# Kernel optimization log

Measured on AMD Instinct MI355X. Metric: run time of the kernel, lower is better.

Reference implementation:

```python
import jax, jax.numpy as jnp
import numpy as np


def _lovasz_softmax_flat(probas, labels):
    # probas: [P, C] softmax probabilities; labels: [P] int class ids
    P, C = probas.shape
    classes = jnp.arange(C)
    # fg[c, p] = 1 if pixel p has ground-truth class c
    fg = (labels[None, :] == classes[:, None]).astype(probas.dtype)      # [C, P]
    errors = jnp.abs(fg - probas.T)                                       # [C, P]
    # sort errors descending per class, permute fg the same way
    order = jnp.argsort(-errors, axis=1)                                  # [C, P]
    errors_sorted = jnp.take_along_axis(errors, order, axis=1)
    fg_sorted = jnp.take_along_axis(fg, order, axis=1)
    # Lovasz gradient of the Jaccard loss w.r.t. sorted errors
    gts = jnp.sum(fg_sorted, axis=1, keepdims=True)                       # [C, 1]
    intersection = gts - jnp.cumsum(fg_sorted, axis=1)
    union = gts + jnp.cumsum(1.0 - fg_sorted, axis=1)
    jaccard = 1.0 - intersection / union                                  # [C, P]
    jaccard = jnp.concatenate([jaccard[:, :1], jaccard[:, 1:] - jaccard[:, :-1]], axis=1)
    # grad is treated as constant w.r.t. probas (matches torch Variable(grad) detach)
    jaccard = jax.lax.stop_gradient(jaccard)
    losses = jnp.sum(errors_sorted * jaccard, axis=1)                     # [C]
    # classes='present': average only over classes present in the labels
    present = (gts[:, 0] > 0).astype(probas.dtype)
    return jnp.sum(losses * present) / jnp.maximum(jnp.sum(present), 1.0)


def reference(input, target):
    B, C, H, W = input.shape
    probas = jax.nn.softmax(input, axis=1)                                # [B, C, H, W]
    probas_flat = probas.transpose(0, 2, 3, 1).reshape(-1, C)             # [P, C]
    labels_flat = target.reshape(-1)                                      # [P]
    return _lovasz_softmax_flat(probas_flat, labels_flat)


def setup_inputs() -> dict:
    key = jax.random.key(0)
    k1, k2 = jax.random.split(key)
    B, C, H, W = 8, 19, 512, 512
    inp = jax.random.normal(k1, (B, C, H, W), dtype=jnp.float32)
    tgt = jax.random.randint(k2, (B, H, W), 0, C, dtype=jnp.int64)
    return {"input": inp, "target": tgt}
```

## Files before the change

### kernel.cpp

```cpp
#include <hip/hip_runtime.h>
#include <stdint.h>


#define C_CLASSES 19
#define NBINS 768
#define HISTWORDS (C_CLASSES * NBINS)
#define HW_SHIFT 18
#define HW_MASK ((1 << HW_SHIFT) - 1)
#define NGROUPS 8

__device__ __forceinline__ void px_process(float* r, float m, int lab,
                                           unsigned int* hist)
{
    float s = 0.f;
#pragma unroll
    for (int c = 0; c < C_CLASSES; ++c) {
        float t = __expf(r[c] - m);
        r[c] = t;
        s += t;
    }
    float scale = (float)(NBINS - 1) * __builtin_amdgcn_rcpf(s);
#pragma unroll
    for (int c = 0; c < C_CLASSES; ++c) {
        int ti = __float2int_rn(r[c] * scale);
        int idx = (c == lab) ? (NBINS - 1 - ti) : ti;
        idx = idx < 0 ? 0 : (idx > NBINS - 1 ? NBINS - 1 : idx);
        atomicAdd(&hist[c * NBINS + idx], (c == lab) ? 0x10001u : 1u);
    }
}

__global__ __launch_bounds__(1024) void k1_hist(
    const float* __restrict__ x, const int* __restrict__ labels,
    unsigned int* __restrict__ copies, int P, int pixPerBlk)
{
    __shared__ unsigned int hist[HISTWORDS];
    int tid = threadIdx.x;
    uint4* h4 = (uint4*)hist;
    for (int i = tid; i < HISTWORDS / 4; i += 1024) h4[i] = make_uint4(0u, 0u, 0u, 0u);
    __syncthreads();

    int base = blockIdx.x * pixPerBlk;
    for (int it = 0; it < pixPerBlk; it += 4096) {
        int pix = base + it + tid * 4;
        if (pix + 3 < P) {
            int img = pix >> HW_SHIFT;
            int rem = pix & HW_MASK;
            const float* xp = x + (((size_t)img * C_CLASSES) << HW_SHIFT) + rem;
            float r0[C_CLASSES], r1[C_CLASSES], r2[C_CLASSES], r3[C_CLASSES];
            float m0 = -3.4e38f, m1 = -3.4e38f, m2 = -3.4e38f, m3 = -3.4e38f;
#pragma unroll
            for (int c = 0; c < C_CLASSES; ++c) {
                float4 v = *reinterpret_cast<const float4*>(xp + ((size_t)c << HW_SHIFT));
                r0[c] = v.x; r1[c] = v.y; r2[c] = v.z; r3[c] = v.w;
                m0 = fmaxf(m0, v.x); m1 = fmaxf(m1, v.y);
                m2 = fmaxf(m2, v.z); m3 = fmaxf(m3, v.w);
            }
            int4 lb = *reinterpret_cast<const int4*>(labels + pix);
            px_process(r0, m0, lb.x, hist);
            px_process(r1, m1, lb.y, hist);
            px_process(r2, m2, lb.z, hist);
            px_process(r3, m3, lb.w, hist);
        } else {
#pragma unroll
            for (int k = 0; k < 4; ++k) {
                int p = pix + k;
                if (p < P) {
                    int img = p >> HW_SHIFT;
                    int rem = p & HW_MASK;
                    const float* xp = x + (((size_t)img * C_CLASSES) << HW_SHIFT) + rem;
                    float r[C_CLASSES];
                    float m = -3.4e38f;
#pragma unroll
                    for (int c = 0; c < C_CLASSES; ++c) {
                        r[c] = xp[(size_t)c << HW_SHIFT];
                        m = fmaxf(m, r[c]);
                    }
                    px_process(r, m, labels[p], hist);
                }
            }
        }
    }
    __syncthreads();
    uint4* dst = (uint4*)(copies + (size_t)blockIdx.x * HISTWORDS);
    const uint4* src = (const uint4*)hist;
    for (int i = tid; i < HISTWORDS / 4; i += 1024) dst[i] = src[i];
}

__global__ __launch_bounds__(256) void k2_reduce(
    const unsigned int* __restrict__ copies,
    int* __restrict__ nPart, int* __restrict__ fPart,
    int* __restrict__ ticket, int ncopies, int cpg)
{
    if (blockIdx.x == 0 && blockIdx.y == 0 && threadIdx.x == 0) *ticket = 0;
    int pos = blockIdx.x * 256 + threadIdx.x;
    int g = blockIdx.y;
    int c0 = g * cpg;
    int c1 = c0 + cpg; if (c1 > ncopies) c1 = ncopies;
    unsigned int sn = 0, sf = 0;
    for (int k = c0; k < c1; ++k) {
        unsigned int w = copies[(size_t)k * HISTWORDS + pos];
        sn += w & 0xFFFFu;
        sf += w >> 16;
    }
    nPart[(size_t)g * HISTWORDS + pos] = (int)sn;
    fPart[(size_t)g * HISTWORDS + pos] = (int)sf;
}

__global__ __launch_bounds__(64) void k3_scan(
    const int* __restrict__ nPart, const int* __restrict__ fPart,
    float* __restrict__ res, int* __restrict__ ticket,
    float* __restrict__ out)
{
    int c = blockIdx.x;
    int lane = threadIdx.x;
    const int PER = NBINS / 64;
    int nl[PER], fl[PER];
    int totN = 0, totF = 0;
#pragma unroll
    for (int i = 0; i < PER; ++i) {
        int j = lane * PER + i;
        int bin = NBINS - 1 - j;
        int pos = c * NBINS + bin;
        int n = 0, f = 0;
#pragma unroll
        for (int g = 0; g < NGROUPS; ++g) {
            n += nPart[g * HISTWORDS + pos];
            f += fPart[g * HISTWORDS + pos];
        }
        nl[i] = n; fl[i] = f; totN += n; totF += f;
    }
    int incN = totN, incF = totF;
    for (int off = 1; off < 64; off <<= 1) {
        int tn = __shfl_up(incN, off);
        int tf = __shfl_up(incF, off);
        if (lane >= off) { incN += tn; incF += tf; }
    }
    int G = __shfl(incF, 63);
    double loss = 0.0;
    if (G > 0) {
        int cumN = incN - totN;
        int cumF = incF - totF;
        double dG = (double)G;
        double Jb = 1.0 - (dG - (double)cumF) / (dG + (double)cumN - (double)cumF);
#pragma unroll
        for (int i = 0; i < PER; ++i) {
            int bin = NBINS - 1 - (lane * PER + i);
            cumN += nl[i]; cumF += fl[i];
            double Ja = 1.0 - (dG - (double)cumF) / (dG + (double)cumN - (double)cumF);
            loss += ((double)bin / (double)(NBINS - 1)) * (Ja - Jb);
            Jb = Ja;
        }
    }
    for (int off = 32; off > 0; off >>= 1)
        loss += __shfl_down(loss, off);
    if (lane == 0) {
        __hip_atomic_store(&res[c], (float)loss, __ATOMIC_RELAXED, __HIP_MEMORY_SCOPE_AGENT);
        __hip_atomic_store(&res[C_CLASSES + c], (float)G, __ATOMIC_RELAXED, __HIP_MEMORY_SCOPE_AGENT);
        int t = __hip_atomic_fetch_add(ticket, 1, __ATOMIC_ACQ_REL, __HIP_MEMORY_SCOPE_AGENT);
        if (t == C_CLASSES - 1) {
            float s = 0.f, cnt = 0.f;
            for (int cc = 0; cc < C_CLASSES; ++cc) {
                float g = __hip_atomic_load(&res[C_CLASSES + cc], __ATOMIC_RELAXED, __HIP_MEMORY_SCOPE_AGENT);
                if (g > 0.f) {
                    s += __hip_atomic_load(&res[cc], __ATOMIC_RELAXED, __HIP_MEMORY_SCOPE_AGENT);
                    cnt += 1.f;
                }
            }
            out[0] = s / fmaxf(cnt, 1.f);
        }
    }
}

extern "C" void kernel_launch(void* const* d_in, const int* in_sizes, int n_in,
                              void* d_out, int out_size, void* d_ws, size_t ws_size,
                              hipStream_t stream)
{
    const float* x = (const float*)d_in[0];
    const int* labels = (const int*)d_in[1];
    float* out = (float*)d_out;
    int P = in_sizes[1];

    const size_t histBytes = (size_t)HISTWORDS * 4;
    const size_t partBytes = (size_t)NGROUPS * HISTWORDS * 4;
    const size_t resBytes = 256;
    const size_t reserved = 2 * partBytes + resBytes + 256;

    int maxCopies = (int)((ws_size > reserved ? ws_size - reserved : 0) / histBytes);
    int ncopies = maxCopies < 256 ? maxCopies : 256;
    if (ncopies < 1) ncopies = 1;
    int pixPerBlk = (P + ncopies - 1) / ncopies;
    pixPerBlk = ((pixPerBlk + 4095) / 4096) * 4096;

    unsigned int* copies = (unsigned int*)d_ws;
    int* nPart = (int*)((char*)d_ws + histBytes * (size_t)ncopies);
    int* fPart = (int*)((char*)nPart + partBytes);
    float* res = (float*)((char*)fPart + partBytes);
    int* ticket = (int*)((char*)res + 160);

    int cpg = (ncopies + NGROUPS - 1) / NGROUPS;

    k1_hist<<<dim3(ncopies), dim3(1024), 0, stream>>>(x, labels, copies, P, pixPerBlk);
    k2_reduce<<<dim3(HISTWORDS / 256, NGROUPS), dim3(256), 0, stream>>>(copies, nPart, fPart, ticket, ncopies, cpg);
    k3_scan<<<dim3(C_CLASSES), dim3(64), 0, stream>>>(nPart, fPart, res, ticket, out);
}
```

Before: 247.7 us.

## Fuse reduce and scan kernels via last-block ticket; drop softmax max subtraction

```diff
diff --git a/kernel.cpp b/kernel.cpp
--- a/kernel.cpp
+++ b/kernel.cpp
@@ -8,58 +8,55 @@
 #define HW_SHIFT 18
 #define HW_MASK ((1 << HW_SHIFT) - 1)
 #define NGROUPS 8
-
-__device__ __forceinline__ void px_process(float* r, float m, int lab,
+#define K2_BLKX (HISTWORDS / 256)
+#define K2_TOTAL (K2_BLKX * NGROUPS)
+
+__device__ __forceinline__ void px_process(const float* r, float s, int lab,
                                            unsigned int* hist)
 {
-    float s = 0.f;
-#pragma unroll
-    for (int c = 0; c < C_CLASSES; ++c) {
-        float t = __expf(r[c] - m);
-        r[c] = t;
-        s += t;
-    }
     float scale = (float)(NBINS - 1) * __builtin_amdgcn_rcpf(s);
 #pragma unroll
     for (int c = 0; c < C_CLASSES; ++c) {
         int ti = __float2int_rn(r[c] * scale);
         int idx = (c == lab) ? (NBINS - 1 - ti) : ti;
-        idx = idx < 0 ? 0 : (idx > NBINS - 1 ? NBINS - 1 : idx);
         atomicAdd(&hist[c * NBINS + idx], (c == lab) ? 0x10001u : 1u);
     }
 }
 
-__global__ __launch_bounds__(1024) void k1_hist(
+__global__ __launch_bounds__(512) void k1_hist(
     const float* __restrict__ x, const int* __restrict__ labels,
-    unsigned int* __restrict__ copies, int P, int pixPerBlk)
+    unsigned int* __restrict__ copies, int* __restrict__ ticket,
+    int P, int pixPerBlk)
 {
     __shared__ unsigned int hist[HISTWORDS];
     int tid = threadIdx.x;
+    if (blockIdx.x == 0 && tid == 0) *ticket = 0;
     uint4* h4 = (uint4*)hist;
-    for (int i = tid; i < HISTWORDS / 4; i += 1024) h4[i] = make_uint4(0u, 0u, 0u, 0u);
+    for (int i = tid; i < HISTWORDS / 4; i += 512) h4[i] = make_uint4(0u, 0u, 0u, 0u);
     __syncthreads();
 
     int base = blockIdx.x * pixPerBlk;
-    for (int it = 0; it < pixPerBlk; it += 4096) {
+    for (int it = 0; it < pixPerBlk; it += 2048) {
         int pix = base + it + tid * 4;
         if (pix + 3 < P) {
             int img = pix >> HW_SHIFT;
             int rem = pix & HW_MASK;
             const float* xp = x + (((size_t)img * C_CLASSES) << HW_SHIFT) + rem;
             float r0[C_CLASSES], r1[C_CLASSES], r2[C_CLASSES], r3[C_CLASSES];
-            float m0 = -3.4e38f, m1 = -3.4e38f, m2 = -3.4e38f, m3 = -3.4e38f;
+            float s0 = 0.f, s1 = 0.f, s2 = 0.f, s3 = 0.f;
 #pragma unroll
             for (int c = 0; c < C_CLASSES; ++c) {
                 float4 v = *reinterpret_cast<const float4*>(xp + ((size_t)c << HW_SHIFT));
-                r0[c] = v.x; r1[c] = v.y; r2[c] = v.z; r3[c] = v.w;
-                m0 = fmaxf(m0, v.x); m1 = fmaxf(m1, v.y);
-                m2 = fmaxf(m2, v.z); m3 = fmaxf(m3, v.w);
+                float e0 = __expf(v.x), e1 = __expf(v.y);
+                float e2 = __expf(v.z), e3 = __expf(v.w);
+                r0[c] = e0; s0 += e0; r1[c] = e1; s1 += e1;
+                r2[c] = e2; s2 += e2; r3[c] = e3; s3 += e3;
             }
             int4 lb = *reinterpret_cast<const int4*>(labels + pix);
-            px_process(r0, m0, lb.x, hist);
-            px_process(r1, m1, lb.y, hist);
-            px_process(r2, m2, lb.z, hist);
-            px_process(r3, m3, lb.w, hist);
+            px_process(r0, s0, lb.x, hist);
+            px_process(r1, s1, lb.y, hist);
+            px_process(r2, s2, lb.z, hist);
+            px_process(r3, s3, lb.w, hist);
         } else {
 #pragma unroll
             for (int k = 0; k < 4; ++k) {
@@ -69,13 +66,13 @@
                     int rem = p & HW_MASK;
                     const float* xp = x + (((size_t)img * C_CLASSES) << HW_SHIFT) + rem;
                     float r[C_CLASSES];
-                    float m = -3.4e38f;
+                    float s = 0.f;
 #pragma unroll
                     for (int c = 0; c < C_CLASSES; ++c) {
-                        r[c] = xp[(size_t)c << HW_SHIFT];
-                        m = fmaxf(m, r[c]);
+                        float e = __expf(xp[(size_t)c << HW_SHIFT]);
+                        r[c] = e; s += e;
                     }
-                    px_process(r, m, labels[p], hist);
+                    px_process(r, s, labels[p], hist);
                 }
             }
         }
@@ -83,91 +80,96 @@
     __syncthreads();
     uint4* dst = (uint4*)(copies + (size_t)blockIdx.x * HISTWORDS);
     const uint4* src = (const uint4*)hist;
-    for (int i = tid; i < HISTWORDS / 4; i += 1024) dst[i] = src[i];
-}
-
-__global__ __launch_bounds__(256) void k2_reduce(
+    for (int i = tid; i < HISTWORDS / 4; i += 512) dst[i] = src[i];
+}
+
+__global__ __launch_bounds__(256) void k2_reduce_scan(
     const unsigned int* __restrict__ copies,
     int* __restrict__ nPart, int* __restrict__ fPart,
-    int* __restrict__ ticket, int ncopies, int cpg)
-{
-    if (blockIdx.x == 0 && blockIdx.y == 0 && threadIdx.x == 0) *ticket = 0;
+    int* __restrict__ ticket, float* __restrict__ out,
+    int ncopies, int cpg)
+{
+    __shared__ float lossS[C_CLASSES], gS[C_CLASSES];
+    __shared__ int lastFlag;
+
     int pos = blockIdx.x * 256 + threadIdx.x;
     int g = blockIdx.y;
-    int c0 = g * cpg;
-    int c1 = c0 + cpg; if (c1 > ncopies) c1 = ncopies;
-    unsigned int sn = 0, sf = 0;
-    for (int k = c0; k < c1; ++k) {
-        unsigned int w = copies[(size_t)k * HISTWORDS + pos];
-        sn += w & 0xFFFFu;
-        sf += w >> 16;
-    }
-    nPart[(size_t)g * HISTWORDS + pos] = (int)sn;
-    fPart[(size_t)g * HISTWORDS + pos] = (int)sf;
-}
-
-__global__ __launch_bounds__(64) void k3_scan(
-    const int* __restrict__ nPart, const int* __restrict__ fPart,
-    float* __restrict__ res, int* __restrict__ ticket,
-    float* __restrict__ out)
-{
-    int c = blockIdx.x;
-    int lane = threadIdx.x;
+    {
+        int c0 = g * cpg;
+        int c1 = c0 + cpg; if (c1 > ncopies) c1 = ncopies;
+        unsigned int sn = 0, sf = 0;
+        for (int k = c0; k < c1; ++k) {
+            unsigned int w = copies[(size_t)k * HISTWORDS + pos];
+            sn += w & 0xFFFFu;
+            sf += w >> 16;
+        }
+        nPart[(size_t)g * HISTWORDS + pos] = (int)sn;
+        fPart[(size_t)g * HISTWORDS + pos] = (int)sf;
+    }
+    __syncthreads();
+    if (threadIdx.x == 0) {
+        __threadfence();
+        int t = __hip_atomic_fetch_add(ticket, 1, __ATOMIC_ACQ_REL,
+                                       __HIP_MEMORY_SCOPE_AGENT);
+        lastFlag = (t == K2_TOTAL - 1) ? 1 : 0;
+    }
+    __syncthreads();
+    if (!lastFlag) return;
+
+    int w = threadIdx.x >> 6;
+    int lane = threadIdx.x & 63;
     const int PER = NBINS / 64;
-    int nl[PER], fl[PER];
-    int totN = 0, totF = 0;
-#pragma unroll
-    for (int i = 0; i < PER; ++i) {
-        int j = lane * PER + i;
-        int bin = NBINS - 1 - j;
-        int pos = c * NBINS + bin;
-        int n = 0, f = 0;
-#pragma unroll
-        for (int g = 0; g < NGROUPS; ++g) {
-            n += nPart[g * HISTWORDS + pos];
-            f += fPart[g * HISTWORDS + pos];
-        }
-        nl[i] = n; fl[i] = f; totN += n; totF += f;
-    }
-    int incN = totN, incF = totF;
-    for (int off = 1; off < 64; off <<= 1) {
-        int tn = __shfl_up(incN, off);
-        int tf = __shfl_up(incF, off);
-        if (lane >= off) { incN += tn; incF += tf; }
-    }
-    int G = __shfl(incF, 63);
-    double loss = 0.0;
-    if (G > 0) {
-        int cumN = incN - totN;
-        int cumF = incF - totF;
-        double dG = (double)G;
-        double Jb = 1.0 - (dG - (double)cumF) / (dG + (double)cumN - (double)cumF);
+    for (int c = w; c < C_CLASSES; c += 4) {
+        int nl[PER], fl[PER];
+        int totN = 0, totF = 0;
 #pragma unroll
         for (int i = 0; i < PER; ++i) {
-            int bin = NBINS - 1 - (lane * PER + i);
-            cumN += nl[i]; cumF += fl[i];
-            double Ja = 1.0 - (dG - (double)cumF) / (dG + (double)cumN - (double)cumF);
-            loss += ((double)bin / (double)(NBINS - 1)) * (Ja - Jb);
-            Jb = Ja;
-        }
-    }
-    for (int off = 32; off > 0; off >>= 1)
-        loss += __shfl_down(loss, off);
-    if (lane == 0) {
-        __hip_atomic_store(&res[c], (float)loss, __ATOMIC_RELAXED, __HIP_MEMORY_SCOPE_AGENT);
-        __hip_atomic_store(&res[C_CLASSES + c], (float)G, __ATOMIC_RELAXED, __HIP_MEMORY_SCOPE_AGENT);
-        int t = __hip_atomic_fetch_add(ticket, 1, __ATOMIC_ACQ_REL, __HIP_MEMORY_SCOPE_AGENT);
-        if (t == C_CLASSES - 1) {
-            float s = 0.f, cnt = 0.f;
-            for (int cc = 0; cc < C_CLASSES; ++cc) {
-                float g = __hip_atomic_load(&res[C_CLASSES + cc], __ATOMIC_RELAXED, __HIP_MEMORY_SCOPE_AGENT);
-                if (g > 0.f) {
-                    s += __hip_atomic_load(&res[cc], __ATOMIC_RELAXED, __HIP_MEMORY_SCOPE_AGENT);
-                    cnt += 1.f;
-                }
-            }
-            out[0] = s / fmaxf(cnt, 1.f);
-        }
+            int j = lane * PER + i;
+            int bin = NBINS - 1 - j;
+            int p = c * NBINS + bin;
+            int n = 0, f = 0;
+#pragma unroll
+            for (int gg = 0; gg < NGROUPS; ++gg) {
+                n += __hip_atomic_load(&nPart[gg * HISTWORDS + p],
+                                       __ATOMIC_RELAXED, __HIP_MEMORY_SCOPE_AGENT);
+                f += __hip_atomic_load(&fPart[gg * HISTWORDS + p],
+                                       __ATOMIC_RELAXED, __HIP_MEMORY_SCOPE_AGENT);
+            }
+            nl[i] = n; fl[i] = f; totN += n; totF += f;
+        }
+        int incN = totN, incF = totF;
+        for (int off = 1; off < 64; off <<= 1) {
+            int tn = __shfl_up(incN, off);
+            int tf = __shfl_up(incF, off);
+            if (lane >= off) { incN += tn; incF += tf; }
+        }
+        int G = __shfl(incF, 63);
+        double loss = 0.0;
+        if (G > 0) {
+            int cumN = incN - totN;
+            int cumF = incF - totF;
+            double dG = (double)G;
+            double Jb = 1.0 - (dG - (double)cumF) / (dG + (double)cumN - (double)cumF);
+#pragma unroll
+            for (int i = 0; i < PER; ++i) {
+                int bin = NBINS - 1 - (lane * PER + i);
+                cumN += nl[i]; cumF += fl[i];
+                double Ja = 1.0 - (dG - (double)cumF) / (dG + (double)cumN - (double)cumF);
+                loss += ((double)bin / (double)(NBINS - 1)) * (Ja - Jb);
+                Jb = Ja;
+            }
+        }
+        for (int off = 32; off > 0; off >>= 1)
+            loss += __shfl_down(loss, off);
+        if (lane == 0) { lossS[c] = (float)loss; gS[c] = (float)G; }
+    }
+    __syncthreads();
+    if (threadIdx.x == 0) {
+        float s = 0.f, cnt = 0.f;
+        for (int c = 0; c < C_CLASSES; ++c) {
+            if (gS[c] > 0.f) { s += lossS[c]; cnt += 1.f; }
+        }
+        out[0] = s / fmaxf(cnt, 1.f);
     }
 }
 
@@ -182,24 +184,21 @@
 
     const size_t histBytes = (size_t)HISTWORDS * 4;
     const size_t partBytes = (size_t)NGROUPS * HISTWORDS * 4;
-    const size_t resBytes = 256;
-    const size_t reserved = 2 * partBytes + resBytes + 256;
+    const size_t reserved = 2 * partBytes + 512;
 
     int maxCopies = (int)((ws_size > reserved ? ws_size - reserved : 0) / histBytes);
     int ncopies = maxCopies < 256 ? maxCopies : 256;
     if (ncopies < 1) ncopies = 1;
     int pixPerBlk = (P + ncopies - 1) / ncopies;
-    pixPerBlk = ((pixPerBlk + 4095) / 4096) * 4096;
+    pixPerBlk = ((pixPerBlk + 2047) / 2048) * 2048;
 
     unsigned int* copies = (unsigned int*)d_ws;
     int* nPart = (int*)((char*)d_ws + histBytes * (size_t)ncopies);
     int* fPart = (int*)((char*)nPart + partBytes);
-    float* res = (float*)((char*)fPart + partBytes);
-    int* ticket = (int*)((char*)res + 160);
+    int* ticket = (int*)((char*)fPart + partBytes);
 
     int cpg = (ncopies + NGROUPS - 1) / NGROUPS;
 
-    k1_hist<<<dim3(ncopies), dim3(1024), 0, stream>>>(x, labels, copies, P, pixPerBlk);
-    k2_reduce<<<dim3(HISTWORDS / 256, NGROUPS), dim3(256), 0, stream>>>(copies, nPart, fPart, ticket, ncopies, cpg);
-    k3_scan<<<dim3(C_CLASSES), dim3(64), 0, stream>>>(nPart, fPart, res, ticket, out);
-}
+    k1_hist<<<dim3(ncopies), dim3(512), 0, stream>>>(x, labels, copies, ticket, P, pixPerBlk);
+    k2_reduce_scan<<<dim3(K2_BLKX, NGROUPS), dim3(256), 0, stream>>>(copies, nPart, fPart, ticket, out, ncopies, cpg);
+}
```

Result: slower. 310.9 us (+25.5%).
